# Kernel tuning notes

Hardware: AMD Instinct MI355X
Metric: run time of the kernel (lower is better)

## Reference

```python
import jax, jax.numpy as jnp
import numpy as np

D_MODEL = 1024
NUM_HEAD = 16
LN_EPS = 1e-5


def _layernorm(x, w, b):
    mu = jnp.mean(x, axis=-1, keepdims=True)
    var = jnp.mean(jnp.square(x - mu), axis=-1, keepdims=True)
    return (x - mu) * jax.lax.rsqrt(var + LN_EPS) * w + b


def setup_inputs() -> dict:
    key = jax.random.key(0)
    ks = jax.random.split(key, 8)
    d = D_MODEL
    s = 1.0 / np.sqrt(d)
    return {
        "text": jax.random.normal(ks[0], (8, 512, d), dtype=jnp.float32),
        "av_feat": jax.random.normal(ks[1], (8, 1024, d), dtype=jnp.float32),
        "tn_w": jnp.ones((d,), jnp.float32),
        "tn_b": jnp.zeros((d,), jnp.float32),
        "an_w": jnp.ones((d,), jnp.float32),
        "an_b": jnp.zeros((d,), jnp.float32),
        "Wq": jax.random.uniform(ks[2], (d, d), jnp.float32, -s, s),
        "bq": jnp.zeros((d,), jnp.float32),
        "Wk": jax.random.uniform(ks[3], (d, d), jnp.float32, -s, s),
        "bk": jnp.zeros((d,), jnp.float32),
        "Wv": jax.random.uniform(ks[4], (d, d), jnp.float32, -s, s),
        "bv": jnp.zeros((d,), jnp.float32),
    }


def reference(text, av_feat, tn_w, tn_b, an_w, an_b, Wq, bq, Wk, bk, Wv, bv):
    bs, num_word, d_model = text.shape
    num_valid = av_feat.shape[1]
    h = NUM_HEAD
    d_k = d_model // h

    t = _layernorm(text, tn_w, tn_b)
    a = _layernorm(av_feat, an_w, an_b)

    # torch Linear: x @ W.T + b
    q = (t @ Wq.T + bq).reshape(bs, num_word, h, d_k)   # b q h d
    k = (a @ Wk.T + bk).reshape(bs, num_valid, h, d_k)  # b k h d
    v = (a @ Wv.T + bv).reshape(bs, num_valid, h, d_k)  # b k h d

    # sigmoid attention (no softmax): scores (bs, num_word, num_valid, num_head)
    attn = jnp.einsum('bqhd,bkhd->bqkh', q, k) / np.sqrt(d_k)
    attn = jax.nn.sigmoid(attn)

    # out = sum over num_valid of attn * v -> (bs, num_word, num_head, d_k)
    out = jnp.einsum('bqkh,bkhd->bqhd', attn, v).reshape(bs, num_word, d_model)
    return out, attn.mean(-1)
```

## Files before the change

### kernel.cpp

```cpp
#include <hip/hip_runtime.h>
#include <hip/hip_bf16.h>

typedef float f32x4 __attribute__((ext_vector_type(4)));
typedef short s16x8 __attribute__((ext_vector_type(8)));

typedef const __attribute__((address_space(1))) unsigned int* gas1_t;
typedef __attribute__((address_space(3))) unsigned int* las3_t;

__device__ __forceinline__ void load_lds16(const void* g, void* l) {
  __builtin_amdgcn_global_load_lds((gas1_t)g, (las3_t)l, 16, 0, 0);
}

__device__ __forceinline__ unsigned short f2bf(float f) {
  union { float f; unsigned u; } v; v.f = f;
  unsigned u = v.u;
  u += 0x7fffu + ((u >> 16) & 1u);
  return (unsigned short)(u >> 16);
}

__global__ __launch_bounds__(256) void ln_bf16_kernel(
    const float* __restrict__ x, const float* __restrict__ w,
    const float* __restrict__ b, unsigned short* __restrict__ out) {
  int row = blockIdx.x;
  int tid = threadIdx.x;
  const float4* xr = (const float4*)(x + (size_t)row * 1024);
  float4 v = xr[tid];
  float s  = v.x + v.y + v.z + v.w;
  float ss = v.x * v.x + v.y * v.y + v.z * v.z + v.w * v.w;
  #pragma unroll
  for (int off = 32; off; off >>= 1) {
    s  += __shfl_down(s, off);
    ss += __shfl_down(ss, off);
  }
  __shared__ float red[8];
  int wid = tid >> 6, lane = tid & 63;
  if (lane == 0) { red[wid] = s; red[wid + 4] = ss; }
  __syncthreads();
  s  = red[0] + red[1] + red[2] + red[3];
  ss = red[4] + red[5] + red[6] + red[7];
  float mu  = s * (1.0f / 1024.0f);
  float var = ss * (1.0f / 1024.0f) - mu * mu;
  float rstd = rsqrtf(var + 1e-5f);
  float4 wv = ((const float4*)w)[tid];
  float4 bv = ((const float4*)b)[tid];
  ushort4 o;
  o.x = f2bf((v.x - mu) * rstd * wv.x + bv.x);
  o.y = f2bf((v.y - mu) * rstd * wv.y + bv.y);
  o.z = f2bf((v.z - mu) * rstd * wv.z + bv.z);
  o.w = f2bf((v.w - mu) * rstd * wv.w + bv.w);
  ((ushort4*)(out + (size_t)row * 1024))[tid] = o;
}

__global__ __launch_bounds__(256) void cvt_bf16_kernel(
    const float* __restrict__ in, unsigned short* __restrict__ out) {
  int i = blockIdx.x * 256 + threadIdx.x;
  float4 v = ((const float4*)in)[i];
  ushort4 o;
  o.x = f2bf(v.x); o.y = f2bf(v.y); o.z = f2bf(v.z); o.w = f2bf(v.w);
  ((ushort4*)out)[i] = o;
}

template <int TRANS>
__global__ __launch_bounds__(256) void gemm_nt_bias_kernel(
    const unsigned short* __restrict__ A, const unsigned short* __restrict__ B,
    const float* __restrict__ bias, unsigned short* __restrict__ C, int M) {
  __shared__ unsigned short As[128 * 32];
  __shared__ unsigned short Bs[128 * 32];
  const int K = 1024, N = 1024;
  int tid = threadIdx.x, lane = tid & 63, wid = tid >> 6;
  int row0 = blockIdx.x * 128, col0 = blockIdx.y * 128;
  int wr = wid >> 1, wc = wid & 1;
  int l15 = lane & 15, kof = (lane >> 4) * 8;
  f32x4 acc[4][4] = {};
  for (int kt = 0; kt < K; kt += 32) {
    #pragma unroll
    for (int r = 0; r < 2; ++r) {
      int ch = wid * 64 + lane + r * 256;
      int rrow = ch >> 2, cc = ch & 3;
      load_lds16(&A[(size_t)(row0 + rrow) * K + kt + cc * 8], &As[ch * 8]);
      load_lds16(&B[(size_t)(col0 + rrow) * K + kt + cc * 8], &Bs[ch * 8]);
    }
    __syncthreads();
    s16x8 af[4], bfr[4];
    #pragma unroll
    for (int m = 0; m < 4; ++m)
      af[m] = *(const s16x8*)&As[(wr * 64 + m * 16 + l15) * 32 + kof];
    #pragma unroll
    for (int n = 0; n < 4; ++n)
      bfr[n] = *(const s16x8*)&Bs[(wc * 64 + n * 16 + l15) * 32 + kof];
    #pragma unroll
    for (int m = 0; m < 4; ++m)
      #pragma unroll
      for (int n = 0; n < 4; ++n)
        acc[m][n] = __builtin_amdgcn_mfma_f32_16x16x32_bf16(af[m], bfr[n], acc[m][n], 0, 0, 0);
    __syncthreads();
  }
  int lg = lane >> 4;
  if (TRANS) {
    int b = row0 >> 10;
    int kbase = (row0 & 1023) + wr * 64 + lg * 4;
    #pragma unroll
    for (int n = 0; n < 4; ++n) {
      int col = col0 + wc * 64 + n * 16 + l15;
      float bb = bias[col];
      unsigned short* cp = C + (size_t)b * 1048576 + (size_t)col * 1024 + kbase;
      #pragma unroll
      for (int m = 0; m < 4; ++m) {
        ushort4 o;
        o.x = f2bf(acc[m][n][0] + bb);
        o.y = f2bf(acc[m][n][1] + bb);
        o.z = f2bf(acc[m][n][2] + bb);
        o.w = f2bf(acc[m][n][3] + bb);
        *(ushort4*)(cp + m * 16) = o;
      }
    }
  } else {
    #pragma unroll
    for (int n = 0; n < 4; ++n) {
      int col = col0 + wc * 64 + n * 16 + l15;
      float bb = bias[col];
      #pragma unroll
      for (int m = 0; m < 4; ++m) {
        #pragma unroll
        for (int j = 0; j < 4; ++j) {
          int row = row0 + wr * 64 + m * 16 + lg * 4 + j;
          C[(size_t)row * N + col] = f2bf(acc[m][n][j] + bb);
        }
      }
    }
  }
}

#define PSTR 40
__global__ __launch_bounds__(1024, 4) void attn_kernel(
    const unsigned short* __restrict__ Q, const unsigned short* __restrict__ K,
    const unsigned short* __restrict__ Vt, float* __restrict__ out,
    float* __restrict__ meanout) {
  __shared__ unsigned short Plds[16 * 32 * PSTR];
  int bid = blockIdx.x;
  int b = bid & 7, qt = bid >> 3;
  int q0 = qt * 32;
  int tid = threadIdx.x, lane = tid & 63, h = tid >> 6;
  int l15 = lane & 15, lg = lane >> 4;

  const unsigned short* Qp = Q + (size_t)(b * 512 + q0) * 1024 + h * 64;
  const unsigned short* Kp = K + (size_t)b * 1048576 + h * 64;
  const unsigned short* Vp = Vt + (size_t)b * 1048576 + (size_t)(h * 64) * 1024;

  s16x8 aq[2][2];
  #pragma unroll
  for (int m = 0; m < 2; ++m)
    #pragma unroll
    for (int ks = 0; ks < 2; ++ks)
      aq[m][ks] = *(const s16x8*)(Qp + (size_t)(m * 16 + l15) * 1024 + ks * 32 + lg * 8);

  f32x4 oacc[2][4] = {};
  unsigned short* Ph = Plds + h * (32 * PSTR);

  for (int kt = 0; kt < 1024; kt += 32) {
    f32x4 s[2][2] = {};
    {
      s16x8 bk[2][2];
      #pragma unroll
      for (int kc = 0; kc < 2; ++kc)
        #pragma unroll
        for (int ks = 0; ks < 2; ++ks)
          bk[kc][ks] = *(const s16x8*)(Kp + (size_t)(kt + kc * 16 + l15) * 1024 + ks * 32 + lg * 8);
      #pragma unroll
      for (int m = 0; m < 2; ++m)
        #pragma unroll
        for (int kc = 0; kc < 2; ++kc) {
          s[m][kc] = __builtin_amdgcn_mfma_f32_16x16x32_bf16(aq[m][0], bk[kc][0], s[m][kc], 0, 0, 0);
          s[m][kc] = __builtin_amdgcn_mfma_f32_16x16x32_bf16(aq[m][1], bk[kc][1], s[m][kc], 0, 0, 0);
        }
    }
    s16x8 bv[4];
    #pragma unroll
    for (int nd = 0; nd < 4; ++nd)
      bv[nd] = *(const s16x8*)(Vp + (size_t)(nd * 16 + l15) * 1024 + kt + lg * 8);

    #pragma unroll
    for (int m = 0; m < 2; ++m)
      #pragma unroll
      for (int kc = 0; kc < 2; ++kc)
        #pragma unroll
        for (int j = 0; j < 4; ++j) {
          float p = __builtin_amdgcn_rcpf(1.0f + __expf(s[m][kc][j] * -0.125f));
          Ph[(m * 16 + lg * 4 + j) * PSTR + kc * 16 + l15] = f2bf(p);
        }
    __syncthreads();

    if (tid < 512) {
      int q = tid >> 4, kc2 = tid & 15;
      const unsigned short* pp = Plds + q * PSTR + kc2 * 2;
      float s0 = 0.f, s1 = 0.f;
      #pragma unroll
      for (int hh = 0; hh < 16; ++hh) {
        unsigned u = *(const unsigned*)(pp + hh * (32 * PSTR));
        union { unsigned u; float f; } lo, hi;
        lo.u = u << 16; hi.u = u & 0xffff0000u;
        s0 += lo.f; s1 += hi.f;
      }
      float2 mo; mo.x = s0 * 0.0625f; mo.y = s1 * 0.0625f;
      *(float2*)&meanout[(size_t)(b * 512 + q0 + q) * 1024 + kt + kc2 * 2] = mo;
    }

    s16x8 pa[2];
    pa[0] = *(const s16x8*)(Ph + l15 * PSTR + lg * 8);
    pa[1] = *(const s16x8*)(Ph + (16 + l15) * PSTR + lg * 8);
    #pragma unroll
    for (int m = 0; m < 2; ++m)
      #pragma unroll
      for (int nd = 0; nd < 4; ++nd)
        oacc[m][nd] = __builtin_amdgcn_mfma_f32_16x16x32_bf16(pa[m], bv[nd], oacc[m][nd], 0, 0, 0);
    __syncthreads();
  }

  #pragma unroll
  for (int m = 0; m < 2; ++m)
    #pragma unroll
    for (int nd = 0; nd < 4; ++nd)
      #pragma unroll
      for (int j = 0; j < 4; ++j) {
        int q = m * 16 + lg * 4 + j, d = h * 64 + nd * 16 + l15;
        out[(size_t)(b * 512 + q0 + q) * 1024 + d] = oacc[m][nd][j];
      }
}

extern "C" void kernel_launch(void* const* d_in, const int* in_sizes, int n_in,
                              void* d_out, int out_size, void* d_ws, size_t ws_size,
                              hipStream_t stream) {
  const float* text = (const float*)d_in[0];
  const float* av   = (const float*)d_in[1];
  const float* tn_w = (const float*)d_in[2];
  const float* tn_b = (const float*)d_in[3];
  const float* an_w = (const float*)d_in[4];
  const float* an_b = (const float*)d_in[5];
  const float* Wq   = (const float*)d_in[6];
  const float* bq   = (const float*)d_in[7];
  const float* Wk   = (const float*)d_in[8];
  const float* bk   = (const float*)d_in[9];
  const float* Wv   = (const float*)d_in[10];
  const float* bv   = (const float*)d_in[11];

  char* ws = (char*)d_ws;
  const size_t MB = 1u << 20;
  unsigned short* Wqb = (unsigned short*)(ws + 0 * MB);
  unsigned short* Wkb = (unsigned short*)(ws + 2 * MB);
  unsigned short* Wvb = (unsigned short*)(ws + 4 * MB);
  unsigned short* Tln = (unsigned short*)(ws + 6 * MB);
  unsigned short* Aln = (unsigned short*)(ws + 14 * MB);
  unsigned short* Qb  = (unsigned short*)(ws + 30 * MB);
  unsigned short* Kb  = (unsigned short*)(ws + 38 * MB);
  unsigned short* Vtb = (unsigned short*)(ws + 54 * MB);

  float* out  = (float*)d_out;
  float* mout = out + (size_t)8 * 512 * 1024;

  ln_bf16_kernel<<<4096, 256, 0, stream>>>(text, tn_w, tn_b, Tln);
  ln_bf16_kernel<<<8192, 256, 0, stream>>>(av, an_w, an_b, Aln);
  cvt_bf16_kernel<<<1024, 256, 0, stream>>>(Wq, Wqb);
  cvt_bf16_kernel<<<1024, 256, 0, stream>>>(Wk, Wkb);
  cvt_bf16_kernel<<<1024, 256, 0, stream>>>(Wv, Wvb);
  dim3 gq(32, 8), gk(64, 8);
  gemm_nt_bias_kernel<0><<<gq, 256, 0, stream>>>(Tln, Wqb, bq, Qb, 4096);
  gemm_nt_bias_kernel<0><<<gk, 256, 0, stream>>>(Aln, Wkb, bk, Kb, 8192);
  gemm_nt_bias_kernel<1><<<gk, 256, 0, stream>>>(Aln, Wvb, bv, Vtb, 8192);
  attn_kernel<<<128, 1024, 0, stream>>>(Qb, Kb, Vtb, out, mout);
}
```

Before: 341.8 us.

## Merge prep and GEMM launches, double-buffer GEMM, retile attention to 16-query blocks

The five layernorm and weight-cast launches become one prep kernel, and the three projection GEMMs become one launch that picks its operands by block index. The GEMM now double-buffers its LDS tiles so the next K-slice load overlaps the current MFMA work. The attention kernel halves the query tile to 16 rows, giving 256 blocks instead of 128 for better CU coverage. It also prefetches K fragments with ping-pong registers, double-buffers the P tile in LDS to drop one barrier per step, and uses exp2 with a folded scale. The cost is that every K/V fragment is read twice as often across blocks, and LDS per GEMM block doubles.

```diff
diff --git a/kernel.cpp b/kernel.cpp
--- a/kernel.cpp
+++ b/kernel.cpp
@@ -1,8 +1,10 @@
 #include <hip/hip_runtime.h>
 #include <hip/hip_bf16.h>
+#include <math.h>
 
 typedef float f32x4 __attribute__((ext_vector_type(4)));
 typedef short s16x8 __attribute__((ext_vector_type(8)));
+typedef unsigned short us;
 
 typedef const __attribute__((address_space(1))) unsigned int* gas1_t;
 typedef __attribute__((address_space(3))) unsigned int* las3_t;
@@ -11,18 +13,37 @@
   __builtin_amdgcn_global_load_lds((gas1_t)g, (las3_t)l, 16, 0, 0);
 }
 
-__device__ __forceinline__ unsigned short f2bf(float f) {
+__device__ __forceinline__ us f2bf(float f) {
   union { float f; unsigned u; } v; v.f = f;
   unsigned u = v.u;
   u += 0x7fffu + ((u >> 16) & 1u);
-  return (unsigned short)(u >> 16);
-}
-
-__global__ __launch_bounds__(256) void ln_bf16_kernel(
-    const float* __restrict__ x, const float* __restrict__ w,
-    const float* __restrict__ b, unsigned short* __restrict__ out) {
-  int row = blockIdx.x;
-  int tid = threadIdx.x;
+  return (us)(u >> 16);
+}
+
+__global__ __launch_bounds__(256) void prep_kernel(
+    const float* __restrict__ text, const float* __restrict__ av,
+    const float* __restrict__ tn_w, const float* __restrict__ tn_b,
+    const float* __restrict__ an_w, const float* __restrict__ an_b,
+    const float* __restrict__ Wq, const float* __restrict__ Wk, const float* __restrict__ Wv,
+    us* __restrict__ Tln, us* __restrict__ Aln,
+    us* __restrict__ Wqb, us* __restrict__ Wkb, us* __restrict__ Wvb) {
+  int id = blockIdx.x, tid = threadIdx.x;
+  if (id >= 12288) {
+    int c = id - 12288;
+    const float* src; us* dst;
+    if (c < 1024)      { src = Wq; dst = Wqb; }
+    else if (c < 2048) { src = Wk; dst = Wkb; c -= 1024; }
+    else               { src = Wv; dst = Wvb; c -= 2048; }
+    int i = c * 256 + tid;
+    float4 v = ((const float4*)src)[i];
+    ushort4 o;
+    o.x = f2bf(v.x); o.y = f2bf(v.y); o.z = f2bf(v.z); o.w = f2bf(v.w);
+    ((ushort4*)dst)[i] = o;
+    return;
+  }
+  const float *x, *w, *b; us* outp; int row;
+  if (id < 4096) { x = text; w = tn_w; b = tn_b; outp = Tln; row = id; }
+  else           { x = av;   w = an_w; b = an_b; outp = Aln; row = id - 4096; }
   const float4* xr = (const float4*)(x + (size_t)row * 1024);
   float4 v = xr[tid];
   float s  = v.x + v.y + v.z + v.w;
@@ -48,62 +69,65 @@
   o.y = f2bf((v.y - mu) * rstd * wv.y + bv.y);
   o.z = f2bf((v.z - mu) * rstd * wv.z + bv.z);
   o.w = f2bf((v.w - mu) * rstd * wv.w + bv.w);
-  ((ushort4*)(out + (size_t)row * 1024))[tid] = o;
-}
-
-__global__ __launch_bounds__(256) void cvt_bf16_kernel(
-    const float* __restrict__ in, unsigned short* __restrict__ out) {
-  int i = blockIdx.x * 256 + threadIdx.x;
-  float4 v = ((const float4*)in)[i];
-  ushort4 o;
-  o.x = f2bf(v.x); o.y = f2bf(v.y); o.z = f2bf(v.z); o.w = f2bf(v.w);
-  ((ushort4*)out)[i] = o;
-}
-
-template <int TRANS>
-__global__ __launch_bounds__(256) void gemm_nt_bias_kernel(
-    const unsigned short* __restrict__ A, const unsigned short* __restrict__ B,
-    const float* __restrict__ bias, unsigned short* __restrict__ C, int M) {
-  __shared__ unsigned short As[128 * 32];
-  __shared__ unsigned short Bs[128 * 32];
+  ((ushort4*)(outp + (size_t)row * 1024))[tid] = o;
+}
+
+__global__ __launch_bounds__(256) void gemm3_kernel(
+    const us* __restrict__ Tln, const us* __restrict__ Aln,
+    const us* __restrict__ Wqb, const us* __restrict__ Wkb, const us* __restrict__ Wvb,
+    const float* __restrict__ bq, const float* __restrict__ bk_, const float* __restrict__ bv_,
+    us* __restrict__ Qb, us* __restrict__ Kb, us* __restrict__ Vtb) {
+  __shared__ us As[2][128 * 32];
+  __shared__ us Bs[2][128 * 32];
   const int K = 1024, N = 1024;
+  int id = blockIdx.x;
+  const us *A, *B; const float* bias; us* C; bool trans = false;
+  int rb, cb;
+  if (id < 256)      { A = Tln; B = Wqb; bias = bq;  C = Qb;  rb = id >> 3; cb = id & 7; }
+  else if (id < 768) { id -= 256; A = Aln; B = Wkb; bias = bk_; C = Kb; rb = id >> 3; cb = id & 7; }
+  else               { id -= 768; A = Aln; B = Wvb; bias = bv_; C = Vtb; rb = id >> 3; cb = id & 7; trans = true; }
+  int row0 = rb * 128, col0 = cb * 128;
   int tid = threadIdx.x, lane = tid & 63, wid = tid >> 6;
-  int row0 = blockIdx.x * 128, col0 = blockIdx.y * 128;
   int wr = wid >> 1, wc = wid & 1;
-  int l15 = lane & 15, kof = (lane >> 4) * 8;
+  int l15 = lane & 15, kof = (lane >> 4) * 8, lg = lane >> 4;
+  int ch0 = wid * 64 + lane, ch1 = ch0 + 256;
+  int r0 = ch0 >> 2, c0 = ch0 & 3, r1 = ch1 >> 2, c1 = ch1 & 3;
+
+#define G3_STAGE(buf, kt)                                                       \
+  { load_lds16(&A[(size_t)(row0 + r0) * K + (kt) + c0 * 8], &As[buf][ch0 * 8]); \
+    load_lds16(&B[(size_t)(col0 + r0) * K + (kt) + c0 * 8], &Bs[buf][ch0 * 8]); \
+    load_lds16(&A[(size_t)(row0 + r1) * K + (kt) + c1 * 8], &As[buf][ch1 * 8]); \
+    load_lds16(&B[(size_t)(col0 + r1) * K + (kt) + c1 * 8], &Bs[buf][ch1 * 8]); }
+
   f32x4 acc[4][4] = {};
+  G3_STAGE(0, 0);
+  __syncthreads();
+  int cur = 0;
   for (int kt = 0; kt < K; kt += 32) {
-    #pragma unroll
-    for (int r = 0; r < 2; ++r) {
-      int ch = wid * 64 + lane + r * 256;
-      int rrow = ch >> 2, cc = ch & 3;
-      load_lds16(&A[(size_t)(row0 + rrow) * K + kt + cc * 8], &As[ch * 8]);
-      load_lds16(&B[(size_t)(col0 + rrow) * K + kt + cc * 8], &Bs[ch * 8]);
-    }
-    __syncthreads();
+    if (kt + 32 < K) G3_STAGE(cur ^ 1, kt + 32);
     s16x8 af[4], bfr[4];
     #pragma unroll
     for (int m = 0; m < 4; ++m)
-      af[m] = *(const s16x8*)&As[(wr * 64 + m * 16 + l15) * 32 + kof];
+      af[m] = *(const s16x8*)&As[cur][(wr * 64 + m * 16 + l15) * 32 + kof];
     #pragma unroll
     for (int n = 0; n < 4; ++n)
-      bfr[n] = *(const s16x8*)&Bs[(wc * 64 + n * 16 + l15) * 32 + kof];
+      bfr[n] = *(const s16x8*)&Bs[cur][(wc * 64 + n * 16 + l15) * 32 + kof];
     #pragma unroll
     for (int m = 0; m < 4; ++m)
       #pragma unroll
       for (int n = 0; n < 4; ++n)
         acc[m][n] = __builtin_amdgcn_mfma_f32_16x16x32_bf16(af[m], bfr[n], acc[m][n], 0, 0, 0);
     __syncthreads();
-  }
-  int lg = lane >> 4;
-  if (TRANS) {
+    cur ^= 1;
+  }
+  if (trans) {
     int b = row0 >> 10;
     int kbase = (row0 & 1023) + wr * 64 + lg * 4;
     #pragma unroll
     for (int n = 0; n < 4; ++n) {
       int col = col0 + wc * 64 + n * 16 + l15;
       float bb = bias[col];
-      unsigned short* cp = C + (size_t)b * 1048576 + (size_t)col * 1024 + kbase;
+      us* cp = C + (size_t)b * 1048576 + (size_t)col * 1024 + kbase;
       #pragma unroll
       for (int m = 0; m < 4; ++m) {
         ushort4 o;
@@ -120,111 +144,115 @@
       int col = col0 + wc * 64 + n * 16 + l15;
       float bb = bias[col];
       #pragma unroll
-      for (int m = 0; m < 4; ++m) {
+      for (int m = 0; m < 4; ++m)
         #pragma unroll
         for (int j = 0; j < 4; ++j) {
           int row = row0 + wr * 64 + m * 16 + lg * 4 + j;
           C[(size_t)row * N + col] = f2bf(acc[m][n][j] + bb);
         }
-      }
     }
   }
+#undef G3_STAGE
 }
 
 #define PSTR 40
+#define PBUF (16 * 16 * PSTR)
 __global__ __launch_bounds__(1024, 4) void attn_kernel(
-    const unsigned short* __restrict__ Q, const unsigned short* __restrict__ K,
-    const unsigned short* __restrict__ Vt, float* __restrict__ out,
+    const us* __restrict__ Q, const us* __restrict__ K,
+    const us* __restrict__ Vt, float* __restrict__ out,
     float* __restrict__ meanout) {
-  __shared__ unsigned short Plds[16 * 32 * PSTR];
+  __shared__ us Plds[2 * PBUF];
   int bid = blockIdx.x;
   int b = bid & 7, qt = bid >> 3;
-  int q0 = qt * 32;
+  int q0 = qt * 16;
   int tid = threadIdx.x, lane = tid & 63, h = tid >> 6;
   int l15 = lane & 15, lg = lane >> 4;
 
-  const unsigned short* Qp = Q + (size_t)(b * 512 + q0) * 1024 + h * 64;
-  const unsigned short* Kp = K + (size_t)b * 1048576 + h * 64;
-  const unsigned short* Vp = Vt + (size_t)b * 1048576 + (size_t)(h * 64) * 1024;
-
-  s16x8 aq[2][2];
+  const us* Qp = Q + (size_t)(b * 512 + q0) * 1024 + h * 64;
+  const us* Kp = K + (size_t)b * 1048576 + h * 64;
+  const us* Vp = Vt + (size_t)b * 1048576 + (size_t)(h * 64) * 1024;
+
+  s16x8 aq0 = *(const s16x8*)(Qp + (size_t)l15 * 1024 + lg * 8);
+  s16x8 aq1 = *(const s16x8*)(Qp + (size_t)l15 * 1024 + 32 + lg * 8);
+
+  f32x4 oacc[4] = {};
+  const float SC = -0.1803368801111244f;
+  const us* Kl = Kp + (size_t)l15 * 1024 + lg * 8;
+  const us* Vl = Vp + (size_t)l15 * 1024 + lg * 8;
+
+  s16x8 bkA[2][2], bkB[2][2];
   #pragma unroll
-  for (int m = 0; m < 2; ++m)
+  for (int kc = 0; kc < 2; ++kc)
     #pragma unroll
     for (int ks = 0; ks < 2; ++ks)
-      aq[m][ks] = *(const s16x8*)(Qp + (size_t)(m * 16 + l15) * 1024 + ks * 32 + lg * 8);
-
-  f32x4 oacc[2][4] = {};
-  unsigned short* Ph = Plds + h * (32 * PSTR);
-
-  for (int kt = 0; kt < 1024; kt += 32) {
-    f32x4 s[2][2] = {};
-    {
-      s16x8 bk[2][2];
-      #pragma unroll
-      for (int kc = 0; kc < 2; ++kc)
-        #pragma unroll
-        for (int ks = 0; ks < 2; ++ks)
-          bk[kc][ks] = *(const s16x8*)(Kp + (size_t)(kt + kc * 16 + l15) * 1024 + ks * 32 + lg * 8);
-      #pragma unroll
-      for (int m = 0; m < 2; ++m)
-        #pragma unroll
-        for (int kc = 0; kc < 2; ++kc) {
-          s[m][kc] = __builtin_amdgcn_mfma_f32_16x16x32_bf16(aq[m][0], bk[kc][0], s[m][kc], 0, 0, 0);
-          s[m][kc] = __builtin_amdgcn_mfma_f32_16x16x32_bf16(aq[m][1], bk[kc][1], s[m][kc], 0, 0, 0);
-        }
+      bkA[kc][ks] = *(const s16x8*)(Kl + (size_t)(kc * 16) * 1024 + ks * 32);
+
+#define ATTN_STEP(KT, BKU, BKP, BUF)                                              \
+  {                                                                               \
+                            \
+    s16x8 bvv[4];                                                                 \
+    _Pragma("unroll")                                                             \
+    for (int nd = 0; nd < 4; ++nd)                                                \
+      bvv[nd] = *(const s16x8*)(Vl + (size_t)(nd * 16) * 1024 + (KT));            \
+                                                                   \
+    f32x4 s0 = {}, s1 = {};                                                       \
+    s0 = __builtin_amdgcn_mfma_f32_16x16x32_bf16(aq0, BKU[0][0], s0, 0, 0, 0);    \
+    s0 = __builtin_amdgcn_mfma_f32_16x16x32_bf16(aq1, BKU[0][1], s0, 0, 0, 0);    \
+    s1 = __builtin_amdgcn_mfma_f32_16x16x32_bf16(aq0, BKU[1][0], s1, 0, 0, 0);    \
+    s1 = __builtin_amdgcn_mfma_f32_16x16x32_bf16(aq1, BKU[1][1], s1, 0, 0, 0);    \
+                                                \
+    if ((KT) + 32 < 1024) {                                                       \
+      _Pragma("unroll")                                                           \
+      for (int kc = 0; kc < 2; ++kc)                                              \
+        _Pragma("unroll")                                                         \
+        for (int ks = 0; ks < 2; ++ks)                                            \
+          BKP[kc][ks] = *(const s16x8*)(Kl + (size_t)((KT) + 32 + kc * 16) * 1024 + ks * 32); \
+    }                                                                             \
+                                              \
+    us* Ph = Plds + (BUF) * PBUF + h * (16 * PSTR);                               \
+    _Pragma("unroll")                                                             \
+    for (int j = 0; j < 4; ++j) {                                                 \
+      float p0 = __builtin_amdgcn_rcpf(1.0f + exp2f(s0[j] * SC));                 \
+      float p1 = __builtin_amdgcn_rcpf(1.0f + exp2f(s1[j] * SC));                 \
+      Ph[(lg * 4 + j) * PSTR + l15]      = f2bf(p0);                              \
+      Ph[(lg * 4 + j) * PSTR + 16 + l15] = f2bf(p1);                              \
+    }                                                                             \
+    __syncthreads();                                                              \
+                    \
+    if (tid < 256) {                                                              \
+      int q = tid >> 4, pr = tid & 15;                                            \
+      const us* pp = Plds + (BUF) * PBUF + q * PSTR + pr * 2;                     \
+      float m0 = 0.f, m1 = 0.f;                                                   \
+      _Pragma("unroll")                                                           \
+      for (int hh = 0; hh < 16; ++hh) {                                           \
+        unsigned u = *(const unsigned*)(pp + hh * (16 * PSTR));                   \
+        union { unsigned u; float f; } lo, hi;                                    \
+        lo.u = u << 16; hi.u = u & 0xffff0000u;                                   \
+        m0 += lo.f; m1 += hi.f;                                                   \
+      }                                                                           \
+      float2 mo; mo.x = m0 * 0.0625f; mo.y = m1 * 0.0625f;                        \
+      *(float2*)&meanout[(size_t)(b * 512 + q0 + q) * 1024 + (KT) + pr * 2] = mo; \
+    }                                                                             \
+                                                                    \
+    s16x8 pa = *(const s16x8*)(Ph + l15 * PSTR + lg * 8);                         \
+    _Pragma("unroll")                                                             \
+    for (int nd = 0; nd < 4; ++nd)                                                \
+      oacc[nd] = __builtin_amdgcn_mfma_f32_16x16x32_bf16(pa, bvv[nd], oacc[nd], 0, 0, 0); \
+  }
+
+  for (int kt = 0; kt < 1024; kt += 64) {
+    ATTN_STEP(kt,      bkA, bkB, 0);
+    ATTN_STEP(kt + 32, bkB, bkA, 1);
+  }
+#undef ATTN_STEP
+
+  #pragma unroll
+  for (int nd = 0; nd < 4; ++nd)
+    #pragma unroll
+    for (int j = 0; j < 4; ++j) {
+      int q = lg * 4 + j, d = h * 64 + nd * 16 + l15;
+      out[(size_t)(b * 512 + q0 + q) * 1024 + d] = oacc[nd][j];
     }
-    s16x8 bv[4];
-    #pragma unroll
-    for (int nd = 0; nd < 4; ++nd)
-      bv[nd] = *(const s16x8*)(Vp + (size_t)(nd * 16 + l15) * 1024 + kt + lg * 8);
-
-    #pragma unroll
-    for (int m = 0; m < 2; ++m)
-      #pragma unroll
-      for (int kc = 0; kc < 2; ++kc)
-        #pragma unroll
-        for (int j = 0; j < 4; ++j) {
-          float p = __builtin_amdgcn_rcpf(1.0f + __expf(s[m][kc][j] * -0.125f));
-          Ph[(m * 16 + lg * 4 + j) * PSTR + kc * 16 + l15] = f2bf(p);
-        }
-    __syncthreads();
-
-    if (tid < 512) {
-      int q = tid >> 4, kc2 = tid & 15;
-      const unsigned short* pp = Plds + q * PSTR + kc2 * 2;
-      float s0 = 0.f, s1 = 0.f;
-      #pragma unroll
-      for (int hh = 0; hh < 16; ++hh) {
-        unsigned u = *(const unsigned*)(pp + hh * (32 * PSTR));
-        union { unsigned u; float f; } lo, hi;
-        lo.u = u << 16; hi.u = u & 0xffff0000u;
-        s0 += lo.f; s1 += hi.f;
-      }
-      float2 mo; mo.x = s0 * 0.0625f; mo.y = s1 * 0.0625f;
-      *(float2*)&meanout[(size_t)(b * 512 + q0 + q) * 1024 + kt + kc2 * 2] = mo;
-    }
-
-    s16x8 pa[2];
-    pa[0] = *(const s16x8*)(Ph + l15 * PSTR + lg * 8);
-    pa[1] = *(const s16x8*)(Ph + (16 + l15) * PSTR + lg * 8);
-    #pragma unroll
-    for (int m = 0; m < 2; ++m)
-      #pragma unroll
-      for (int nd = 0; nd < 4; ++nd)
-        oacc[m][nd] = __builtin_amdgcn_mfma_f32_16x16x32_bf16(pa[m], bv[nd], oacc[m][nd], 0, 0, 0);
-    __syncthreads();
-  }
-
-  #pragma unroll
-  for (int m = 0; m < 2; ++m)
-    #pragma unroll
-    for (int nd = 0; nd < 4; ++nd)
-      #pragma unroll
-      for (int j = 0; j < 4; ++j) {
-        int q = m * 16 + lg * 4 + j, d = h * 64 + nd * 16 + l15;
-        out[(size_t)(b * 512 + q0 + q) * 1024 + d] = oacc[m][nd][j];
-      }
 }
 
 extern "C" void kernel_launch(void* const* d_in, const int* in_sizes, int n_in,
@@ -245,26 +273,21 @@
 
   char* ws = (char*)d_ws;
   const size_t MB = 1u << 20;
-  unsigned short* Wqb = (unsigned short*)(ws + 0 * MB);
-  unsigned short* Wkb = (unsigned short*)(ws + 2 * MB);
-  unsigned short* Wvb = (unsigned short*)(ws + 4 * MB);
-  unsigned short* Tln = (unsigned short*)(ws + 6 * MB);
-  unsigned short* Aln = (unsigned short*)(ws + 14 * MB);
-  unsigned short* Qb  = (unsigned short*)(ws + 30 * MB);
-  unsigned short* Kb  = (unsigned short*)(ws + 38 * MB);
-  unsigned short* Vtb = (unsigned short*)(ws + 54 * MB);
+  us* Wqb = (us*)(ws + 0 * MB);
+  us* Wkb = (us*)(ws + 2 * MB);
+  us* Wvb = (us*)(ws + 4 * MB);
+  us* Tln = (us*)(ws + 6 * MB);
+  us* Aln = (us*)(ws + 14 * MB);
+  us* Qb  = (us*)(ws + 30 * MB);
+  us* Kb  = (us*)(ws + 38 * MB);
+  us* Vtb = (us*)(ws + 54 * MB);
 
   float* out  = (float*)d_out;
   float* mout = out + (size_t)8 * 512 * 1024;
 
-  ln_bf16_kernel<<<4096, 256, 0, stream>>>(text, tn_w, tn_b, Tln);
-  ln_bf16_kernel<<<8192, 256, 0, stream>>>(av, an_w, an_b, Aln);
-  cvt_bf16_kernel<<<1024, 256, 0, stream>>>(Wq, Wqb);
-  cvt_bf16_kernel<<<1024, 256, 0, stream>>>(Wk, Wkb);
-  cvt_bf16_kernel<<<1024, 256, 0, stream>>>(Wv, Wvb);
-  dim3 gq(32, 8), gk(64, 8);
-  gemm_nt_bias_kernel<0><<<gq, 256, 0, stream>>>(Tln, Wqb, bq, Qb, 4096);
-  gemm_nt_bias_kernel<0><<<gk, 256, 0, stream>>>(Aln, Wkb, bk, Kb, 8192);
-  gemm_nt_bias_kernel<1><<<gk, 256, 0, stream>>>(Aln, Wvb, bv, Vtb, 8192);
-  attn_kernel<<<128, 1024, 0, stream>>>(Qb, Kb, Vtb, out, mout);
-}
+  prep_kernel<<<15360, 256, 0, stream>>>(text, av, tn_w, tn_b, an_w, an_b,
+                                         Wq, Wk, Wv, Tln, Aln, Wqb, Wkb, Wvb);
+  gemm3_kernel<<<1280, 256, 0, stream>>>(Tln, Aln, Wqb, Wkb, Wvb,
+                                         bq, bk, bv, Qb, Kb, Vtb);
+  attn_kernel<<<256, 1024, 0, stream>>>(Qb, Kb, Vtb, out, mout);
+}
```

Result: faster. 323.1 us (-5.5%).
